# Kernel tuning notes

Hardware: AMD Instinct MI355X
Metric: run time of the kernel (lower is better)

The kernel has to match this reference:

```python
import jax, jax.numpy as jnp
import numpy as np

EMBED = 1024
HEADS = 16
DH = EMBED // HEADS
B, S = 2, 2048


def setup_inputs() -> dict:
    key = jax.random.key(0)
    ks = jax.random.split(key, 12)
    inp = {
        "k": jax.random.normal(ks[0], (B, S, EMBED), jnp.float32),
        "q": jax.random.normal(ks[1], (B, S, EMBED), jnp.float32),
        "v": jax.random.normal(ks[2], (B, S, EMBED), jnp.float32),
        "mask": jax.random.randint(ks[3], (B, 1, S, S), 0, 2, jnp.int32),
        # per-head projections (shared across heads, as in the torch module)
        "Wk": jax.random.normal(ks[4], (DH, DH), jnp.float32) / np.sqrt(DH),
        "bk": jnp.zeros((DH,), jnp.float32),
        "Wq": jax.random.normal(ks[5], (DH, DH), jnp.float32) / np.sqrt(DH),
        "bq": jnp.zeros((DH,), jnp.float32),
        "Wv": jax.random.normal(ks[6], (DH, DH), jnp.float32) / np.sqrt(DH),
        "bv": jnp.zeros((DH,), jnp.float32),
        "Wo": jax.random.normal(ks[7], (EMBED, EMBED), jnp.float32) / np.sqrt(EMBED),
        "bo": jnp.zeros((EMBED,), jnp.float32),
    }
    return inp


def reference(k, q, v, mask, Wk, bk, Wq, bq, Wv, bv, Wo, bo):
    b, s, _ = k.shape
    sq = q.shape[1]
    # [B,S,H,dh]
    kh = k.reshape(b, s, HEADS, DH)
    qh = q.reshape(b, sq, HEADS, DH)
    vh = v.reshape(b, s, HEADS, DH)
    # per-head linear (weight shared across heads): x @ W.T + b
    kh = kh @ Wk.T + bk
    qh = qh @ Wq.T + bq
    vh = vh @ Wv.T + bv
    # scores [B,H,Sq,Sk]
    product = jnp.einsum("bqhd,bkhd->bhqk", qh, kh)
    # masked_fill BEFORE scaling, as in the original
    product = jnp.where(mask == 0, jnp.float32(-1e20), product)
    product = product / np.sqrt(DH)
    scores = jax.nn.softmax(product, axis=-1)
    ctx = jnp.einsum("bhqk,bkhd->bqhd", scores, vh).reshape(b, sq, EMBED)
    return ctx @ Wo.T + bo
```

## Files before the change

### kernel.cpp

```cpp
#include <hip/hip_runtime.h>
#include <hip/hip_bf16.h>
#include <math.h>

#define EMBED 1024
#define HEADS 16
#define DH    64
#define BATCH 2
#define SEQ   2048

typedef __attribute__((ext_vector_type(8))) short bf16x8;
typedef __attribute__((ext_vector_type(4))) short bf16x4;
typedef __attribute__((ext_vector_type(4))) float f32x4;
typedef unsigned long long u64;
typedef __attribute__((ext_vector_type(2))) unsigned long long u64x2;

#define QSCALE 0.1803368801111244f

static __device__ __forceinline__ unsigned short f2bf(float x) {
    unsigned u = __builtin_bit_cast(unsigned, x);
    return (unsigned short)((u + 0x7fffu + ((u >> 16) & 1u)) >> 16);
}
static __device__ __forceinline__ unsigned pk2bf(float a, float b) {
    union { __hip_bfloat162 h2; unsigned u; } c;
    c.h2 = __float22bfloat162_rn(make_float2(a, b));
    return c.u;
}
static __device__ __forceinline__ float fexp2(float x) {
#if __has_builtin(__builtin_amdgcn_exp2f)
    return __builtin_amdgcn_exp2f(x);
#else
    float r; asm("v_exp_f32 %0, %1" : "=v"(r) : "v"(x)); return r;
#endif
}
static __device__ __forceinline__ void gl_lds16(const void* g, void* l) {
    __builtin_amdgcn_global_load_lds(
        (const __attribute__((address_space(1))) void*)g,
        (__attribute__((address_space(3))) void*)l, 16, 0, 0);
}
static __device__ __forceinline__ bf16x8 cvt8(const float* p) {
    float4 a = ((const float4*)p)[0];
    float4 b = ((const float4*)p)[1];
    union { unsigned u[4]; bf16x8 v; } c;
    c.u[0] = pk2bf(a.x, a.y); c.u[1] = pk2bf(a.z, a.w);
    c.u[2] = pk2bf(b.x, b.y); c.u[3] = pk2bf(b.z, b.w);
    return c.v;
}

__global__ __launch_bounds__(256) void proj_mfma(
    const float* __restrict__ q, const float* __restrict__ k, const float* __restrict__ v,
    const float* __restrict__ Wq, const float* __restrict__ bq,
    const float* __restrict__ Wk, const float* __restrict__ bk,
    const float* __restrict__ Wv, const float* __restrict__ bv,
    unsigned short* __restrict__ qh, unsigned short* __restrict__ kh,
    unsigned short* __restrict__ vt,
    const int* __restrict__ mask, u64* __restrict__ bits,
    const float* __restrict__ Wo, unsigned short* __restrict__ Wob)
{
    const int blk   = blockIdx.x;
    const int which = blockIdx.y;
    const int t     = threadIdx.x;

    if (which == 3) {
        if (blk < 512) {
            const int idx = blk * 256 + t;
            const int4* src = (const int4*)(mask + (size_t)idx * 64);
            u64 wb = 0;
#pragma unroll
            for (int u = 0; u < 16; ++u) {
                int4 m = src[u];
                u64 nib = (m.x != 0 ? 1ull : 0) | (m.y != 0 ? 2ull : 0) |
                          (m.z != 0 ? 4ull : 0) | (m.w != 0 ? 8ull : 0);
                wb |= nib << (u * 4);
            }
            bits[idx] = wb;
        } else {
            const int i = ((blk - 512) * 256 + t) * 8;
            float4 a = ((const float4*)(Wo + i))[0];
            float4 b = ((const float4*)(Wo + i))[1];
            unsigned o32[4] = {pk2bf(a.x, a.y), pk2bf(a.z, a.w),
                               pk2bf(b.x, b.y), pk2bf(b.z, b.w)};
            *(uint4*)(Wob + i) = *(uint4*)o32;
        }
        return;
    }

    const float* x; const float* W; const float* bias;
    if (which == 0)      { x = q; W = Wq; bias = bq; }
    else if (which == 1) { x = k; W = Wk; bias = bk; }
    else                 { x = v; W = Wv; bias = bv; }

    __shared__ unsigned short Ws[64 * 72];

    const int w    = t >> 6;
    const int lane = t & 63;
    const int l15  = lane & 15;
    const int quad = lane >> 4;

    const int sr = t >> 2, sp = t & 3;
    {
        const float* wsrc = W + (size_t)sr * 64 + sp * 16;
        unsigned o32[8];
#pragma unroll
        for (int u4 = 0; u4 < 4; ++u4) {
            float4 a = ((const float4*)wsrc)[u4];
            o32[u4 * 2 + 0] = pk2bf(a.x, a.y);
            o32[u4 * 2 + 1] = pk2bf(a.z, a.w);
        }
        *(uint4*)&Ws[sr * 72 + sp * 16]     = *(uint4*)&o32[0];
        *(uint4*)&Ws[sr * 72 + sp * 16 + 8] = *(uint4*)&o32[4];
    }

    if (which == 2) {
        const int bh = blk >> 5;
        const int st = blk & 31;
        const int b  = bh >> 4, h = bh & 15;
        const int c  = w * 16 + l15;
        const int s  = st * 64 + c;
        const int cp = (c & 32) + ((c & 12) << 1) + ((c & 16) >> 2) + (c & 3);

        const float* xrow = x + ((size_t)(b * SEQ + s)) * EMBED + h * DH;
        const bf16x8 bx0 = cvt8(xrow + quad * 8);
        const bf16x8 bx1 = cvt8(xrow + 32 + quad * 8);

        __syncthreads();

#pragma unroll
        for (int nt = 0; nt < 4; ++nt) {
            bf16x8 aw0 = *(const bf16x8*)&Ws[(nt * 16 + l15) * 72 + quad * 8];
            bf16x8 aw1 = *(const bf16x8*)&Ws[(nt * 16 + l15) * 72 + 32 + quad * 8];
            f32x4 a = {0, 0, 0, 0};
            a = __builtin_amdgcn_mfma_f32_16x16x32_bf16(aw0, bx0, a, 0, 0, 0);
            a = __builtin_amdgcn_mfma_f32_16x16x32_bf16(aw1, bx1, a, 0, 0, 0);
#pragma unroll
            for (int r = 0; r < 4; ++r) {
                const int d = nt * 16 + quad * 4 + r;
                vt[((size_t)bh * DH + d) * SEQ + st * 64 + cp] = f2bf(a[r] + bias[d]);
            }
        }
        return;
    }

    const float oscale = (which == 0) ? QSCALE : 1.0f;
    unsigned short* out = (which == 0) ? qh : kh;

    const float* xrow = x + ((size_t)blk * 64 + w * 16 + l15) * 64;
    const bf16x8 bx0 = cvt8(xrow + quad * 8);
    const bf16x8 bx1 = cvt8(xrow + 32 + quad * 8);

    __syncthreads();

    const int bs = blk * 4 + w;
    const int b = bs >> 11, s = bs & 2047;
    unsigned short* obase = out + (((size_t)b * HEADS + l15) * SEQ + s) * DH + quad * 4;

#pragma unroll
    for (int nt = 0; nt < 4; ++nt) {
        bf16x8 aw0 = *(const bf16x8*)&Ws[(nt * 16 + l15) * 72 + quad * 8];
        bf16x8 aw1 = *(const bf16x8*)&Ws[(nt * 16 + l15) * 72 + 32 + quad * 8];
        f32x4 a = {0, 0, 0, 0};
        a = __builtin_amdgcn_mfma_f32_16x16x32_bf16(aw0, bx0, a, 0, 0, 0);
        a = __builtin_amdgcn_mfma_f32_16x16x32_bf16(aw1, bx1, a, 0, 0, 0);
        const int d0 = nt * 16 + quad * 4;
        const float4 bb = *(const float4*)&bias[d0];
        unsigned o2[2] = {pk2bf((a[0] + bb.x) * oscale, (a[1] + bb.y) * oscale),
                          pk2bf((a[2] + bb.z) * oscale, (a[3] + bb.w) * oscale)};
        *(uint2*)(obase + nt * 16) = *(uint2*)o2;
    }
}

__global__ __launch_bounds__(256, 2) void attn_kernel(
    const unsigned short* __restrict__ qh, const unsigned short* __restrict__ kh,
    const unsigned short* __restrict__ vt, const u64* __restrict__ mbits,
    unsigned short* __restrict__ ctx)
{
    const int bid = blockIdx.x;
    const int bh  = bid & 31;
    const int q0  = (bid >> 5) * 128;
    const int b   = bh >> 4;

    __shared__ unsigned char smem[65536];

    const int t    = threadIdx.x;
    const int w    = t >> 6;
    const int lane = t & 63;
    const int l15  = lane & 15;
    const int quad = lane >> 4;

    const int srow   = lane >> 3;
    const int schunk = (lane & 7) ^ srow;

    bf16x8 qf[2][2];
#pragma unroll
    for (int g = 0; g < 2; ++g) {
        const unsigned short* qb =
            qh + ((size_t)bh * SEQ + q0 + w * 32 + g * 16 + l15) * DH + quad * 8;
        qf[g][0] = *(const bf16x8*)qb;
        qf[g][1] = *(const bf16x8*)(qb + 32);
    }

    f32x4 O[2][4];
#pragma unroll
    for (int g = 0; g < 2; ++g)
#pragma unroll
        for (int dt = 0; dt < 4; ++dt) O[g][dt] = f32x4{0, 0, 0, 0};
    f32x4 Osum[2] = {f32x4{0, 0, 0, 0}, f32x4{0, 0, 0, 0}};
    const bf16x8 ones8 = {(short)0x3F80, (short)0x3F80, (short)0x3F80, (short)0x3F80,
                          (short)0x3F80, (short)0x3F80, (short)0x3F80, (short)0x3F80};

    const unsigned short* kbase = kh + (size_t)bh * SEQ * DH
                                  + (size_t)srow * DH + schunk * 8;
    const unsigned short* vbase = vt + (size_t)bh * DH * SEQ
                                  + (size_t)srow * SEQ + schunk * 8;
    const u64* mrow0 = mbits + ((size_t)b * SEQ + q0 + w * 32 + l15) * (SEQ / 64);
    const u64* mrow1 = mrow0 + 16 * (SEQ / 64);

    auto stage = [&](int kp, unsigned char* buf) {
#pragma unroll
        for (int j = 0; j < 8; ++j) {
            const int idx = w * 8 + j;
            if (idx < 16) {
                const int u = idx >> 3, i = idx & 7;
                gl_lds16(kbase + ((size_t)kp * 128 + u * 64 + i * 8) * DH,
                         buf + u * 8192 + i * 1024);
            } else {
                const int u = (idx - 16) >> 3, i = (idx - 16) & 7;
                gl_lds16(vbase + kp * 128 + u * 64 + (size_t)i * 8 * SEQ,
                         buf + 16384 + u * 8192 + i * 1024);
            }
        }
    };

    stage(0, smem);
    u64 pm00 = mrow0[0], pm01 = mrow0[1], pm10 = mrow1[0], pm11 = mrow1[1];
    __syncthreads();

    for (int it = 0; it < 16; ++it) {
        u64x2 nA, nB;
        if (it < 15) {
            stage(it + 1, smem + ((it + 1) & 1) * 32768);
            nA = *(const u64x2*)&mrow0[2 * it + 2];
            nB = *(const u64x2*)&mrow1[2 * it + 2];
            asm volatile("s_waitcnt vmcnt(10)" ::: "memory");
        } else {
            asm volatile("s_waitcnt vmcnt(0)" ::: "memory");
        }
        __builtin_amdgcn_s_barrier();
        __builtin_amdgcn_sched_barrier(0);

        const unsigned char* buf = smem + (it & 1) * 32768;

        __builtin_amdgcn_s_setprio(1);
#pragma unroll
        for (int u = 0; u < 2; ++u) {
            const unsigned short* KtH = (const unsigned short*)(buf + u * 8192);
            const unsigned short* VtH = (const unsigned short*)(buf + 16384 + u * 8192);
            const u64 mq0 = (u ? pm01 : pm00) >> (quad * 4);
            const u64 mq1 = (u ? pm11 : pm10) >> (quad * 4);

            unsigned pw[2][2][4];
            const int rx = l15 & 7;
#pragma unroll
            for (int st = 0; st < 4; ++st) {
                const int r = st * 16 + l15;
                bf16x8 kf0 = *(const bf16x8*)&KtH[r * 64 + ((quad ^ rx)) * 8];
                bf16x8 kf1 = *(const bf16x8*)&KtH[r * 64 + ((quad ^ rx) ^ 4) * 8];
#pragma unroll
                for (int g = 0; g < 2; ++g) {
                    f32x4 sa = {0, 0, 0, 0};
                    sa = __builtin_amdgcn_mfma_f32_16x16x32_bf16(kf0, qf[g][0], sa, 0, 0, 0);
                    sa = __builtin_amdgcn_mfma_f32_16x16x32_bf16(kf1, qf[g][1], sa, 0, 0, 0);
                    const unsigned nib =
                        (unsigned)((g ? mq1 : mq0) >> (st * 16)) & 0xFu;
                    float p0 = (nib & 1u) ? fexp2(sa[0]) : 0.f;
                    float p1 = (nib & 2u) ? fexp2(sa[1]) : 0.f;
                    float p2 = (nib & 4u) ? fexp2(sa[2]) : 0.f;
                    float p3 = (nib & 8u) ? fexp2(sa[3]) : 0.f;
                    pw[g][st >> 1][2 * (st & 1)]     = pk2bf(p0, p1);
                    pw[g][st >> 1][2 * (st & 1) + 1] = pk2bf(p2, p3);
                }
            }
            bf16x8 p8[2][2];
#pragma unroll
            for (int g = 0; g < 2; ++g)
#pragma unroll
                for (int sp = 0; sp < 2; ++sp) {
                    union { unsigned u4[4]; bf16x8 v; } pu;
                    pu.u4[0] = pw[g][sp][0]; pu.u4[1] = pw[g][sp][1];
                    pu.u4[2] = pw[g][sp][2]; pu.u4[3] = pw[g][sp][3];
                    p8[g][sp] = pu.v;
                    Osum[g] = __builtin_amdgcn_mfma_f32_16x16x32_bf16(
                        p8[g][sp], ones8, Osum[g], 0, 0, 0);
                }

#pragma unroll
            for (int dt = 0; dt < 4; ++dt) {
                const int d = dt * 16 + l15;
                const int dx = l15 & 7;
#pragma unroll
                for (int sp = 0; sp < 2; ++sp) {
                    const int ch = (sp * 4 + quad) ^ dx;
                    bf16x8 vb = *(const bf16x8*)&VtH[d * 64 + ch * 8];
                    O[0][dt] = __builtin_amdgcn_mfma_f32_16x16x32_bf16(
                        p8[0][sp], vb, O[0][dt], 0, 0, 0);
                    O[1][dt] = __builtin_amdgcn_mfma_f32_16x16x32_bf16(
                        p8[1][sp], vb, O[1][dt], 0, 0, 0);
                }
            }
        }
        __builtin_amdgcn_s_setprio(0);
        __builtin_amdgcn_sched_barrier(0);
        __builtin_amdgcn_s_barrier();

        if (it < 15) { pm00 = nA[0]; pm01 = nA[1]; pm10 = nB[0]; pm11 = nB[1]; }
    }

#pragma unroll
    for (int g = 0; g < 2; ++g) {
        float inv[4];
#pragma unroll
        for (int r = 0; r < 4; ++r) inv[r] = 1.0f / Osum[g][r];
#pragma unroll
        for (int r = 0; r < 4; ++r) {
            const int row = q0 + w * 32 + g * 16 + quad * 4 + r;
            unsigned short* dst = ctx + ((size_t)bh * SEQ + row) * DH + l15;
#pragma unroll
            for (int dt = 0; dt < 4; ++dt)
                dst[dt * 16] = f2bf(O[g][dt][r] * inv[r]);
        }
    }
}

__global__ __launch_bounds__(256, 3) void outproj_mfma(
    const unsigned short* __restrict__ ctx, const unsigned short* __restrict__ Wob,
    const float* __restrict__ bo, float* __restrict__ out)
{
    const int n0 = blockIdx.x * 64;
    const int m0 = blockIdx.y * 128;
    const int b  = m0 / SEQ;
    const int s0 = m0 % SEQ;

    __shared__ unsigned char smem[49152];

    const int t    = threadIdx.x;
    const int w    = t >> 6;
    const int lane = t & 63;
    const int l15  = lane & 15;
    const int quad = lane >> 4;
    const int srow   = lane >> 3;
    const int schunk = (lane & 7) ^ srow;

    const unsigned short* abase = ctx + ((size_t)b * HEADS * SEQ + s0 + srow) * DH + schunk * 8;
    const unsigned short* wbase = Wob + (size_t)(n0 + srow) * EMBED + schunk * 8;

    f32x4 acc[8];
#pragma unroll
    for (int mt = 0; mt < 8; ++mt) acc[mt] = f32x4{0, 0, 0, 0};

    auto stage = [&](int kt, unsigned char* buf) {
#pragma unroll
        for (int j = 0; j < 6; ++j) {
            const int idx = w * 6 + j;
            if (idx < 16)
                gl_lds16(abase + (size_t)kt * SEQ * DH + (size_t)idx * 8 * DH,
                         buf + idx * 1024);
            else
                gl_lds16(wbase + (size_t)(idx - 16) * 8 * EMBED + kt * 64,
                         buf + 16384 + (idx - 16) * 1024);
        }
    };

    stage(0, smem);
    __syncthreads();

    for (int kt = 0; kt < 16; ++kt) {
        if (kt < 15) stage(kt + 1, smem + ((kt + 1) & 1) * 24576);

        const unsigned char* buf = smem + (kt & 1) * 24576;
        const unsigned short* At = (const unsigned short*)buf;
        const unsigned short* Wt = (const unsigned short*)(buf + 16384);
        const int rx = l15 & 7;
        const int c0 = ((quad ^ rx)) * 8;

        __builtin_amdgcn_s_setprio(1);
        bf16x8 bf0 = *(const bf16x8*)&Wt[(w * 16 + l15) * 64 + c0];
        bf16x8 bf1 = *(const bf16x8*)&Wt[(w * 16 + l15) * 64 + (c0 ^ 32)];
#pragma unroll
        for (int mt = 0; mt < 8; ++mt) {
            bf16x8 af0 = *(const bf16x8*)&At[(mt * 16 + l15) * 64 + c0];
            bf16x8 af1 = *(const bf16x8*)&At[(mt * 16 + l15) * 64 + (c0 ^ 32)];
            acc[mt] = __builtin_amdgcn_mfma_f32_16x16x32_bf16(af0, bf0, acc[mt], 0, 0, 0);
            acc[mt] = __builtin_amdgcn_mfma_f32_16x16x32_bf16(af1, bf1, acc[mt], 0, 0, 0);
        }
        __builtin_amdgcn_s_setprio(0);
        __syncthreads();
    }

    const float bv = bo[n0 + w * 16 + l15];
#pragma unroll
    for (int mt = 0; mt < 8; ++mt) {
#pragma unroll
        for (int r = 0; r < 4; ++r) {
            out[(size_t)(m0 + mt * 16 + quad * 4 + r) * EMBED + n0 + w * 16 + l15] =
                acc[mt][r] + bv;
        }
    }
}

extern "C" void kernel_launch(void* const* d_in, const int* in_sizes, int n_in,
                              void* d_out, int out_size, void* d_ws, size_t ws_size,
                              hipStream_t stream) {
    const float* k    = (const float*)d_in[0];
    const float* q    = (const float*)d_in[1];
    const float* v    = (const float*)d_in[2];
    const int*   mask = (const int*)  d_in[3];
    const float* Wk   = (const float*)d_in[4];
    const float* bk   = (const float*)d_in[5];
    const float* Wq   = (const float*)d_in[6];
    const float* bq   = (const float*)d_in[7];
    const float* Wv   = (const float*)d_in[8];
    const float* bv   = (const float*)d_in[9];
    const float* Wo   = (const float*)d_in[10];
    const float* bo   = (const float*)d_in[11];
    float* out = (float*)d_out;

    const size_t TEN = (size_t)BATCH * HEADS * SEQ * DH;
    unsigned short* qh_bf = (unsigned short*)d_ws;
    unsigned short* kh_bf = qh_bf + TEN;
    unsigned short* vt_bf = kh_bf + TEN;
    unsigned short* ctxb  = vt_bf + TEN;
    unsigned short* Wob   = ctxb + TEN;
    u64*            mbits = (u64*)(Wob + EMBED * EMBED);

    proj_mfma<<<dim3(1024, 4), 256, 0, stream>>>(
        q, k, v, Wq, bq, Wk, bk, Wv, bv,
        qh_bf, kh_bf, vt_bf, mask, mbits, Wo, Wob);
    attn_kernel<<<dim3((SEQ / 128) * BATCH * HEADS), 256, 0, stream>>>(
        qh_bf, kh_bf, vt_bf, mbits, ctxb);
    outproj_mfma<<<dim3(EMBED / 64, BATCH * SEQ / 128), 256, 0, stream>>>(
        ctxb, Wob, bo, out);
}
```

Baseline: 210.6 us.

## Halve attention query tile to 64 rows and raise occupancy to four blocks

```diff
diff --git a/kernel.cpp b/kernel.cpp
--- a/kernel.cpp
+++ b/kernel.cpp
@@ -168,17 +168,17 @@
     }
 }
 
-__global__ __launch_bounds__(256, 2) void attn_kernel(
+__global__ __launch_bounds__(256, 4) void attn_kernel(
     const unsigned short* __restrict__ qh, const unsigned short* __restrict__ kh,
     const unsigned short* __restrict__ vt, const u64* __restrict__ mbits,
     unsigned short* __restrict__ ctx)
 {
     const int bid = blockIdx.x;
     const int bh  = bid & 31;
-    const int q0  = (bid >> 5) * 128;
+    const int q0  = (bid >> 5) * 64;
     const int b   = bh >> 4;
 
-    __shared__ unsigned char smem[65536];
+    __shared__ unsigned char smem[32768];
 
     const int t    = threadIdx.x;
     const int w    = t >> 6;
@@ -189,21 +189,14 @@
     const int srow   = lane >> 3;
     const int schunk = (lane & 7) ^ srow;
 
-    bf16x8 qf[2][2];
-#pragma unroll
-    for (int g = 0; g < 2; ++g) {
-        const unsigned short* qb =
-            qh + ((size_t)bh * SEQ + q0 + w * 32 + g * 16 + l15) * DH + quad * 8;
-        qf[g][0] = *(const bf16x8*)qb;
-        qf[g][1] = *(const bf16x8*)(qb + 32);
-    }
-
-    f32x4 O[2][4];
-#pragma unroll
-    for (int g = 0; g < 2; ++g)
-#pragma unroll
-        for (int dt = 0; dt < 4; ++dt) O[g][dt] = f32x4{0, 0, 0, 0};
-    f32x4 Osum[2] = {f32x4{0, 0, 0, 0}, f32x4{0, 0, 0, 0}};
+    const unsigned short* qb = qh + ((size_t)bh * SEQ + q0 + w * 16 + l15) * DH + quad * 8;
+    const bf16x8 qf0 = *(const bf16x8*)qb;
+    const bf16x8 qf1 = *(const bf16x8*)(qb + 32);
+
+    f32x4 O[4];
+#pragma unroll
+    for (int dt = 0; dt < 4; ++dt) O[dt] = f32x4{0, 0, 0, 0};
+    f32x4 Osum = {0, 0, 0, 0};
     const bf16x8 ones8 = {(short)0x3F80, (short)0x3F80, (short)0x3F80, (short)0x3F80,
                           (short)0x3F80, (short)0x3F80, (short)0x3F80, (short)0x3F80};
 
@@ -211,122 +204,99 @@
                                   + (size_t)srow * DH + schunk * 8;
     const unsigned short* vbase = vt + (size_t)bh * DH * SEQ
                                   + (size_t)srow * SEQ + schunk * 8;
-    const u64* mrow0 = mbits + ((size_t)b * SEQ + q0 + w * 32 + l15) * (SEQ / 64);
-    const u64* mrow1 = mrow0 + 16 * (SEQ / 64);
-
-    auto stage = [&](int kp, unsigned char* buf) {
-#pragma unroll
-        for (int j = 0; j < 8; ++j) {
-            const int idx = w * 8 + j;
-            if (idx < 16) {
-                const int u = idx >> 3, i = idx & 7;
-                gl_lds16(kbase + ((size_t)kp * 128 + u * 64 + i * 8) * DH,
-                         buf + u * 8192 + i * 1024);
-            } else {
-                const int u = (idx - 16) >> 3, i = (idx - 16) & 7;
-                gl_lds16(vbase + kp * 128 + u * 64 + (size_t)i * 8 * SEQ,
-                         buf + 16384 + u * 8192 + i * 1024);
-            }
+    const u64* mrow = mbits + ((size_t)b * SEQ + q0 + w * 16 + l15) * (SEQ / 64);
+
+    auto stage = [&](int kt, unsigned char* buf) {
+#pragma unroll
+        for (int j = 0; j < 4; ++j) {
+            const int idx = w * 4 + j;
+            if (idx < 8)
+                gl_lds16(kbase + ((size_t)kt * 64 + idx * 8) * DH, buf + idx * 1024);
+            else
+                gl_lds16(vbase + kt * 64 + (size_t)(idx - 8) * 8 * SEQ,
+                         buf + 8192 + (idx - 8) * 1024);
         }
     };
 
     stage(0, smem);
-    u64 pm00 = mrow0[0], pm01 = mrow0[1], pm10 = mrow1[0], pm11 = mrow1[1];
+    u64 pm = mrow[0];
     __syncthreads();
 
-    for (int it = 0; it < 16; ++it) {
-        u64x2 nA, nB;
-        if (it < 15) {
-            stage(it + 1, smem + ((it + 1) & 1) * 32768);
-            nA = *(const u64x2*)&mrow0[2 * it + 2];
-            nB = *(const u64x2*)&mrow1[2 * it + 2];
-            asm volatile("s_waitcnt vmcnt(10)" ::: "memory");
+    for (int it = 0; it < 32; ++it) {
+        u64 nM = 0;
+        if (it < 31) {
+            stage(it + 1, smem + ((it + 1) & 1) * 16384);
+            nM = mrow[it + 1];
+            asm volatile("s_waitcnt vmcnt(5)" ::: "memory");
         } else {
             asm volatile("s_waitcnt vmcnt(0)" ::: "memory");
         }
         __builtin_amdgcn_s_barrier();
         __builtin_amdgcn_sched_barrier(0);
 
-        const unsigned char* buf = smem + (it & 1) * 32768;
+        const unsigned char* buf = smem + (it & 1) * 16384;
+        const unsigned short* KtH = (const unsigned short*)buf;
+        const unsigned short* VtH = (const unsigned short*)(buf + 8192);
+        const u64 mq = pm >> (quad * 4);
 
         __builtin_amdgcn_s_setprio(1);
-#pragma unroll
-        for (int u = 0; u < 2; ++u) {
-            const unsigned short* KtH = (const unsigned short*)(buf + u * 8192);
-            const unsigned short* VtH = (const unsigned short*)(buf + 16384 + u * 8192);
-            const u64 mq0 = (u ? pm01 : pm00) >> (quad * 4);
-            const u64 mq1 = (u ? pm11 : pm10) >> (quad * 4);
-
-            unsigned pw[2][2][4];
-            const int rx = l15 & 7;
-#pragma unroll
-            for (int st = 0; st < 4; ++st) {
-                const int r = st * 16 + l15;
-                bf16x8 kf0 = *(const bf16x8*)&KtH[r * 64 + ((quad ^ rx)) * 8];
-                bf16x8 kf1 = *(const bf16x8*)&KtH[r * 64 + ((quad ^ rx) ^ 4) * 8];
-#pragma unroll
-                for (int g = 0; g < 2; ++g) {
-                    f32x4 sa = {0, 0, 0, 0};
-                    sa = __builtin_amdgcn_mfma_f32_16x16x32_bf16(kf0, qf[g][0], sa, 0, 0, 0);
-                    sa = __builtin_amdgcn_mfma_f32_16x16x32_bf16(kf1, qf[g][1], sa, 0, 0, 0);
-                    const unsigned nib =
-                        (unsigned)((g ? mq1 : mq0) >> (st * 16)) & 0xFu;
-                    float p0 = (nib & 1u) ? fexp2(sa[0]) : 0.f;
-                    float p1 = (nib & 2u) ? fexp2(sa[1]) : 0.f;
-                    float p2 = (nib & 4u) ? fexp2(sa[2]) : 0.f;
-                    float p3 = (nib & 8u) ? fexp2(sa[3]) : 0.f;
-                    pw[g][st >> 1][2 * (st & 1)]     = pk2bf(p0, p1);
-                    pw[g][st >> 1][2 * (st & 1) + 1] = pk2bf(p2, p3);
-                }
-            }
-            bf16x8 p8[2][2];
-#pragma unroll
-            for (int g = 0; g < 2; ++g)
-#pragma unroll
-                for (int sp = 0; sp < 2; ++sp) {
-                    union { unsigned u4[4]; bf16x8 v; } pu;
-                    pu.u4[0] = pw[g][sp][0]; pu.u4[1] = pw[g][sp][1];
-                    pu.u4[2] = pw[g][sp][2]; pu.u4[3] = pw[g][sp][3];
-                    p8[g][sp] = pu.v;
-                    Osum[g] = __builtin_amdgcn_mfma_f32_16x16x32_bf16(
-                        p8[g][sp], ones8, Osum[g], 0, 0, 0);
-                }
-
-#pragma unroll
-            for (int dt = 0; dt < 4; ++dt) {
-                const int d = dt * 16 + l15;
-                const int dx = l15 & 7;
-#pragma unroll
-                for (int sp = 0; sp < 2; ++sp) {
-                    const int ch = (sp * 4 + quad) ^ dx;
-                    bf16x8 vb = *(const bf16x8*)&VtH[d * 64 + ch * 8];
-                    O[0][dt] = __builtin_amdgcn_mfma_f32_16x16x32_bf16(
-                        p8[0][sp], vb, O[0][dt], 0, 0, 0);
-                    O[1][dt] = __builtin_amdgcn_mfma_f32_16x16x32_bf16(
-                        p8[1][sp], vb, O[1][dt], 0, 0, 0);
-                }
+
+        unsigned pw[2][4];
+        const int rx = l15 & 7;
+#pragma unroll
+        for (int st = 0; st < 4; ++st) {
+            const int r = st * 16 + l15;
+            bf16x8 kf0 = *(const bf16x8*)&KtH[r * 64 + ((quad ^ rx)) * 8];
+            bf16x8 kf1 = *(const bf16x8*)&KtH[r * 64 + ((quad ^ rx) ^ 4) * 8];
+            f32x4 sa = {0, 0, 0, 0};
+            sa = __builtin_amdgcn_mfma_f32_16x16x32_bf16(kf0, qf0, sa, 0, 0, 0);
+            sa = __builtin_amdgcn_mfma_f32_16x16x32_bf16(kf1, qf1, sa, 0, 0, 0);
+            const unsigned nib = (unsigned)(mq >> (st * 16)) & 0xFu;
+            float p0 = (nib & 1u) ? fexp2(sa[0]) : 0.f;
+            float p1 = (nib & 2u) ? fexp2(sa[1]) : 0.f;
+            float p2 = (nib & 4u) ? fexp2(sa[2]) : 0.f;
+            float p3 = (nib & 8u) ? fexp2(sa[3]) : 0.f;
+            pw[st >> 1][2 * (st & 1)]     = pk2bf(p0, p1);
+            pw[st >> 1][2 * (st & 1) + 1] = pk2bf(p2, p3);
+        }
+        bf16x8 p8[2];
+#pragma unroll
+        for (int sp = 0; sp < 2; ++sp) {
+            union { unsigned u4[4]; bf16x8 v; } pu;
+            pu.u4[0] = pw[sp][0]; pu.u4[1] = pw[sp][1];
+            pu.u4[2] = pw[sp][2]; pu.u4[3] = pw[sp][3];
+            p8[sp] = pu.v;
+            Osum = __builtin_amdgcn_mfma_f32_16x16x32_bf16(p8[sp], ones8, Osum, 0, 0, 0);
+        }
+
+#pragma unroll
+        for (int dt = 0; dt < 4; ++dt) {
+            const int d = dt * 16 + l15;
+            const int dx = l15 & 7;
+#pragma unroll
+            for (int sp = 0; sp < 2; ++sp) {
+                const int ch = (sp * 4 + quad) ^ dx;
+                bf16x8 vb = *(const bf16x8*)&VtH[d * 64 + ch * 8];
+                O[dt] = __builtin_amdgcn_mfma_f32_16x16x32_bf16(p8[sp], vb, O[dt], 0, 0, 0);
             }
         }
         __builtin_amdgcn_s_setprio(0);
         __builtin_amdgcn_sched_barrier(0);
         __builtin_amdgcn_s_barrier();
 
-        if (it < 15) { pm00 = nA[0]; pm01 = nA[1]; pm10 = nB[0]; pm11 = nB[1]; }
-    }
-
-#pragma unroll
-    for (int g = 0; g < 2; ++g) {
-        float inv[4];
-#pragma unroll
-        for (int r = 0; r < 4; ++r) inv[r] = 1.0f / Osum[g][r];
-#pragma unroll
-        for (int r = 0; r < 4; ++r) {
-            const int row = q0 + w * 32 + g * 16 + quad * 4 + r;
-            unsigned short* dst = ctx + ((size_t)bh * SEQ + row) * DH + l15;
-#pragma unroll
-            for (int dt = 0; dt < 4; ++dt)
-                dst[dt * 16] = f2bf(O[g][dt][r] * inv[r]);
-        }
+        if (it < 31) pm = nM;
+    }
+
+    float inv[4];
+#pragma unroll
+    for (int r = 0; r < 4; ++r) inv[r] = 1.0f / Osum[r];
+#pragma unroll
+    for (int r = 0; r < 4; ++r) {
+        const int row = q0 + w * 16 + quad * 4 + r;
+        unsigned short* dst = ctx + ((size_t)bh * SEQ + row) * DH + l15;
+#pragma unroll
+        for (int dt = 0; dt < 4; ++dt)
+            dst[dt * 16] = f2bf(O[dt][r] * inv[r]);
     }
 }
 
@@ -434,7 +404,7 @@
     proj_mfma<<<dim3(1024, 4), 256, 0, stream>>>(
         q, k, v, Wq, bq, Wk, bk, Wv, bv,
         qh_bf, kh_bf, vt_bf, mask, mbits, Wo, Wob);
-    attn_kernel<<<dim3((SEQ / 128) * BATCH * HEADS), 256, 0, stream>>>(
+    attn_kernel<<<dim3((SEQ / 64) * BATCH * HEADS), 256, 0, stream>>>(
         qh_bf, kh_bf, vt_bf, mbits, ctxb);
     outproj_mfma<<<dim3(EMBED / 64, BATCH * SEQ / 128), 256, 0, stream>>>(
         ctxb, Wob, bo, out);
```

New measurement: 217.3 us. +3.2%, slower.
